# Kernel tuning notes

Hardware: AMD Instinct MI355X
Metric: run time of the kernel (lower is better)

Reference implementation:

```python
import jax, jax.numpy as jnp
import numpy as np

N, E, H, R = 32768, 524288, 128, 64
INV_SQRT_3 = 1.0 / np.sqrt(3.0)
INV_SQRT_H = 1.0 / np.sqrt(float(H))
INV_SQRT_2 = 1.0 / np.sqrt(2.0)


def scaled_silu(x):
    return jax.nn.silu(x) * (1.0 / 0.6)


def setup_inputs() -> dict:
    key = jax.random.key(0)
    ks = jax.random.split(key, 16)
    s = 0.05
    return {
        "x": jax.random.normal(ks[0], (N, H), jnp.float32),
        "vec": jax.random.normal(ks[1], (N, 3, H), jnp.float32),
        "edge_index": jax.random.randint(ks[2], (2, E), 0, N),
        "edge_embed": jax.random.normal(ks[3], (E, R), jnp.float32),
        "edge_vec": jax.random.normal(ks[4], (E, 3), jnp.float32),
        # message layer params
        "ln_g": jnp.ones((H,), jnp.float32),
        "ln_b": jnp.zeros((H,), jnp.float32),
        "W1": jax.random.normal(ks[5], (H, H), jnp.float32) * s,
        "b1": jnp.zeros((H,), jnp.float32),
        "W2": jax.random.normal(ks[6], (H, 3 * H), jnp.float32) * s,
        "b2": jnp.zeros((3 * H,), jnp.float32),
        "Wr": jax.random.normal(ks[7], (R, 3 * H), jnp.float32) * s,
        "br": jnp.zeros((3 * H,), jnp.float32),
        # update layer params
        "Wv": jax.random.normal(ks[8], (H, 2 * H), jnp.float32) * s,
        "Wu1": jax.random.normal(ks[9], (2 * H, H), jnp.float32) * s,
        "bu1": jnp.zeros((H,), jnp.float32),
        "Wu2": jax.random.normal(ks[10], (H, 3 * H), jnp.float32) * s,
        "bu2": jnp.zeros((3 * H,), jnp.float32),
    }


def _layernorm(x, g, b, eps=1e-5):
    mu = jnp.mean(x, axis=-1, keepdims=True)
    var = jnp.mean((x - mu) ** 2, axis=-1, keepdims=True)
    return (x - mu) * jax.lax.rsqrt(var + eps) * g + b


def _painn(x, vec, edge_index, edge_embed, edge_vec,
           ln_g, ln_b, W1, b1, W2, b2, Wr, br, Wv, Wu1, bu1, Wu2, bu2):
    src, dst = edge_index[0], edge_index[1]
    # --- message ---
    xh = scaled_silu(_layernorm(x, ln_g, ln_b) @ W1 + b1) @ W2 + b2  # [N,3H]
    rbfh = edge_embed @ Wr + br                                       # [E,3H]
    m = xh[src] * rbfh                                                # [E,3H]
    xh1, xh2, xh3 = jnp.split(m, 3, axis=-1)
    xh2 = xh2 * INV_SQRT_3
    vec_msg = (vec[src] * xh2[:, None, :] + xh3[:, None, :] * edge_vec[:, :, None]) * INV_SQRT_H  # [E,3,H]
    dx = jax.ops.segment_sum(xh1, dst, num_segments=N)
    dvec = jax.ops.segment_sum(vec_msg, dst, num_segments=N)
    x = (x + dx) * INV_SQRT_2
    vec = vec + dvec
    # --- update ---
    vproj = jnp.einsum('nch,hk->nck', vec, Wv)  # [N,3,2H]
    vec1, vec2 = jnp.split(vproj, 2, axis=-1)
    vec_dot = jnp.sum(vec1 * vec2, axis=1) * INV_SQRT_H  # [N,H]
    vec2_norm = jnp.sqrt(jnp.sum(vec2 ** 2, axis=-2) + 1e-8)  # [N,H]
    h = scaled_silu(jnp.concatenate([x, vec2_norm], axis=-1) @ Wu1 + bu1) @ Wu2 + bu2
    xv1, xv2, xv3 = jnp.split(h, 3, axis=-1)
    dx = (xv1 + xv2 * vec_dot) * INV_SQRT_2
    dvec = xv3[:, None, :] * vec1
    return vec + dvec, x + dx


def reference(x, vec, edge_index, edge_embed, edge_vec,
              ln_g, ln_b, W1, b1, W2, b2, Wr, br, Wv, Wu1, bu1, Wu2, bu2):
    return _painn(x, vec, edge_index, edge_embed, edge_vec,
                  ln_g, ln_b, W1, b1, W2, b2, Wr, br, Wv, Wu1, bu1, Wu2, bu2)
```

## Files before the change

### kernel.cpp

```cpp
#include <hip/hip_runtime.h>
#include <cstdint>
#include <cstddef>

#define NN 32768
#define NE 524288
#define H  128
#define H3 384
#define RB 64
#define EB 16
#define NPB 4
#define EEST 72
#define MSTRIDE 388
#define AST 136

#define INV_SQRT_3 0.5773502691896258f
#define INV_SQRT_H 0.08838834764831845f
#define INV_SQRT_2 0.7071067811865476f

typedef __attribute__((ext_vector_type(8))) short short8;
typedef __attribute__((ext_vector_type(4))) float f32x4;

__device__ __forceinline__ float scaled_silu(float v) {
    return v * (1.0f / 0.6f) / (1.0f + __expf(-v));
}
__device__ __forceinline__ short f2bf(float f) {
    uint32_t u = __float_as_uint(f);
    uint32_t r = (u + 0x7FFFu + ((u >> 16) & 1u)) >> 16;
    return (short)r;
}
__device__ __forceinline__ float bf2f(short s) {
    return __uint_as_float(((uint32_t)(uint16_t)s) << 16);
}

__global__ __launch_bounds__(256) void cvtT_kernel(const float* __restrict__ W,
        short* __restrict__ WT, int K, int M) {
    int i = blockIdx.x * 256 + threadIdx.x;
    int k = i / M, m = i % M;
    WT[(size_t)m * K + k] = f2bf(W[(size_t)k * M + m]);
}

__global__ __launch_bounds__(256) void veccvt_kernel(const float* __restrict__ v,
        short* __restrict__ vb) {
    int i = blockIdx.x * 256 + threadIdx.x;
    float4 a = ((const float4*)v)[i];
    short4 s4; s4.x = f2bf(a.x); s4.y = f2bf(a.y); s4.z = f2bf(a.z); s4.w = f2bf(a.w);
    ((short4*)vb)[i] = s4;
}

__global__ __launch_bounds__(256) void ln_kernel(const float* __restrict__ x,
        const float* __restrict__ g, const float* __restrict__ b,
        float* __restrict__ t) {
    int row  = blockIdx.x * 4 + (threadIdx.x >> 6);
    int lane = threadIdx.x & 63;
    const float* xr = x + (size_t)row * H;
    float v0 = xr[lane], v1 = xr[lane + 64];
    float s = v0 + v1;
#pragma unroll
    for (int off = 32; off; off >>= 1) s += __shfl_xor(s, off, 64);
    float mu = s * (1.0f / 128.0f);
    float d0 = v0 - mu, d1 = v1 - mu;
    float q = d0 * d0 + d1 * d1;
#pragma unroll
    for (int off = 32; off; off >>= 1) q += __shfl_xor(q, off, 64);
    float rs = rsqrtf(q * (1.0f / 128.0f) + 1e-5f);
    float* tr = t + (size_t)row * H;
    tr[lane]      = d0 * rs * g[lane]      + b[lane];
    tr[lane + 64] = d1 * rs * g[lane + 64] + b[lane + 64];
}

__global__ __launch_bounds__(256) void g1_mfma(const float* __restrict__ t,
        const short* __restrict__ W1T, const float* __restrict__ b1,
        short* __restrict__ h1_bf) {
    __shared__ short A_l[64 * AST];
    __shared__ short B_l[128 * AST];
    int tid = threadIdx.x;
    int w = tid >> 6, l = tid & 63, lm = l & 15, q = l >> 4;
    int r0 = blockIdx.x * 64;
    const float4* ag = (const float4*)(t + (size_t)r0 * H);
#pragma unroll
    for (int i = 0; i < 8; ++i) {
        int idx = tid + 256 * i;
        float4 a = ag[idx];
        int row = idx >> 5, c4 = idx & 31;
        short4 s4; s4.x = f2bf(a.x); s4.y = f2bf(a.y); s4.z = f2bf(a.z); s4.w = f2bf(a.w);
        *(short4*)&A_l[row * AST + c4 * 4] = s4;
    }
    const short8* wg = (const short8*)W1T;
#pragma unroll
    for (int i = 0; i < 8; ++i) {
        int idx = tid + 256 * i;
        int row = idx >> 4, c8 = idx & 15;
        *(short8*)&B_l[row * AST + c8 * 8] = wg[idx];
    }
    __syncthreads();
    short8 bf[2][4];
#pragma unroll
    for (int c = 0; c < 2; ++c)
#pragma unroll
        for (int ks = 0; ks < 4; ++ks)
            bf[c][ks] = *(const short8*)&B_l[((2 * w + c) * 16 + lm) * AST + ks * 32 + q * 8];
    f32x4 acc[4][2];
#pragma unroll
    for (int rt = 0; rt < 4; ++rt) { acc[rt][0] = (f32x4){0.f,0.f,0.f,0.f}; acc[rt][1] = (f32x4){0.f,0.f,0.f,0.f}; }
#pragma unroll
    for (int ks = 0; ks < 4; ++ks)
#pragma unroll
        for (int rt = 0; rt < 4; ++rt) {
            short8 a = *(const short8*)&A_l[(rt * 16 + lm) * AST + ks * 32 + q * 8];
            acc[rt][0] = __builtin_amdgcn_mfma_f32_16x16x32_bf16(a, bf[0][ks], acc[rt][0], 0, 0, 0);
            acc[rt][1] = __builtin_amdgcn_mfma_f32_16x16x32_bf16(a, bf[1][ks], acc[rt][1], 0, 0, 0);
        }
#pragma unroll
    for (int c = 0; c < 2; ++c) {
        int col = (2 * w + c) * 16 + lm;
        float bb = b1[col];
#pragma unroll
        for (int rt = 0; rt < 4; ++rt)
#pragma unroll
            for (int r = 0; r < 4; ++r) {
                int R = r0 + rt * 16 + q * 4 + r;
                h1_bf[(size_t)R * H + col] = f2bf(scaled_silu(acc[rt][c][r] + bb));
            }
    }
}

__global__ __launch_bounds__(256) void g2_mfma(const short* __restrict__ h1_bf,
        const short* __restrict__ W2T, const float* __restrict__ b2,
        short* __restrict__ xh_bf) {
    __shared__ short A_l[64 * AST];
    __shared__ short B_l[128 * AST];
    int tid = threadIdx.x;
    int w = tid >> 6, l = tid & 63, lm = l & 15, q = l >> 4;
    int r0 = blockIdx.x * 64;
    const short8* ag = (const short8*)(h1_bf + (size_t)r0 * H);
#pragma unroll
    for (int i = 0; i < 4; ++i) {
        int idx = tid + 256 * i;
        int row = idx >> 4, c8 = idx & 15;
        *(short8*)&A_l[row * AST + c8 * 8] = ag[idx];
    }
    for (int s = 0; s < 3; ++s) {
        __syncthreads();
        const short8* wg = (const short8*)(W2T + (size_t)s * 128 * 128);
#pragma unroll
        for (int i = 0; i < 8; ++i) {
            int idx = tid + 256 * i;
            int row = idx >> 4, c8 = idx & 15;
            *(short8*)&B_l[row * AST + c8 * 8] = wg[idx];
        }
        __syncthreads();
        short8 bf[2][4];
#pragma unroll
        for (int c = 0; c < 2; ++c)
#pragma unroll
            for (int ks = 0; ks < 4; ++ks)
                bf[c][ks] = *(const short8*)&B_l[((2 * w + c) * 16 + lm) * AST + ks * 32 + q * 8];
        f32x4 acc[4][2];
#pragma unroll
        for (int rt = 0; rt < 4; ++rt) { acc[rt][0] = (f32x4){0.f,0.f,0.f,0.f}; acc[rt][1] = (f32x4){0.f,0.f,0.f,0.f}; }
#pragma unroll
        for (int ks = 0; ks < 4; ++ks)
#pragma unroll
            for (int rt = 0; rt < 4; ++rt) {
                short8 a = *(const short8*)&A_l[(rt * 16 + lm) * AST + ks * 32 + q * 8];
                acc[rt][0] = __builtin_amdgcn_mfma_f32_16x16x32_bf16(a, bf[0][ks], acc[rt][0], 0, 0, 0);
                acc[rt][1] = __builtin_amdgcn_mfma_f32_16x16x32_bf16(a, bf[1][ks], acc[rt][1], 0, 0, 0);
            }
#pragma unroll
        for (int c = 0; c < 2; ++c) {
            int col = (2 * w + c) * 16 + lm;
            float bb = b2[s * H + col];
#pragma unroll
            for (int rt = 0; rt < 4; ++rt)
#pragma unroll
                for (int r = 0; r < 4; ++r) {
                    int R = r0 + rt * 16 + q * 4 + r;
                    xh_bf[(size_t)R * H3 + s * H + col] = f2bf(acc[rt][c][r] + bb);
                }
        }
    }
}

__global__ __launch_bounds__(256) void hist_kernel(const int* __restrict__ eidx,
        int* __restrict__ hist) {
    int e = blockIdx.x * 256 + threadIdx.x;
    atomicAdd(&hist[eidx[NE + e]], 1);
}

__global__ __launch_bounds__(1024) void scan_kernel(const int* __restrict__ hist,
        int* __restrict__ row_ptr, int* __restrict__ cursor) {
    __shared__ int sc[1024];
    int t = threadIdx.x;
    int base = t * 32;
    int v[32];
    int s = 0;
#pragma unroll
    for (int i = 0; i < 32; ++i) {
        int tmp = hist[base + i];
        v[i] = s;
        s += tmp;
    }
    sc[t] = s;
    __syncthreads();
    for (int off = 1; off < 1024; off <<= 1) {
        int a = sc[t];
        int b = (t >= off) ? sc[t - off] : 0;
        __syncthreads();
        sc[t] = a + b;
        __syncthreads();
    }
    int excl = sc[t] - s;
#pragma unroll
    for (int i = 0; i < 32; ++i) {
        int val = excl + v[i];
        row_ptr[base + i] = val;
        cursor[base + i] = val;
    }
    if (t == 0) row_ptr[32768] = NE;
}

__global__ __launch_bounds__(256) void scatter_kernel(const int* __restrict__ eidx,
        const float* __restrict__ evec, int* __restrict__ cursor,
        int* __restrict__ perm, int* __restrict__ srcs_s, int* __restrict__ dsts_s,
        float* __restrict__ ev_s) {
    int e = blockIdx.x * 256 + threadIdx.x;
    int d = eidx[NE + e];
    int pos = atomicAdd(&cursor[d], 1);
    perm[pos]   = e;
    srcs_s[pos] = eidx[e];
    dsts_s[pos] = d;
    ev_s[pos * 3 + 0] = evec[e * 3 + 0];
    ev_s[pos * 3 + 1] = evec[e * 3 + 1];
    ev_s[pos * 3 + 2] = evec[e * 3 + 2];
}

__global__ __launch_bounds__(256) void wrt_kernel(const float* __restrict__ Wr,
        short* __restrict__ WrT16) {
    int i = blockIdx.x * 256 + threadIdx.x;
    int n = i >> 6, k = i & 63;
    WrT16[i] = f2bf(Wr[(size_t)k * H3 + n]);
}

__global__ __launch_bounds__(384) void edge_mfma_kernel(
        const int* __restrict__ row_ptr, const int* __restrict__ perm,
        const int* __restrict__ srcs_s, const int* __restrict__ dsts_s,
        const float* __restrict__ ev_s, const float* __restrict__ eembed,
        const short* __restrict__ WrT16, const float* __restrict__ br,
        const short* __restrict__ xh_bf, const short* __restrict__ vec_bf,
        float* __restrict__ dx_out, float* __restrict__ dvec_out) {
    __shared__ float accdx[NPB * H];
    __shared__ float accdv[NPB * H3];
    __shared__ short eeL[EB * EEST];
    __shared__ float mst[EB * MSTRIDE];
    __shared__ int   sSrc[EB];
    __shared__ int   sLd[EB];
    __shared__ float sEv[EB][3];
    int j = threadIdx.x;
    int w = j >> 6, l = j & 63;
    int lm = l & 15, q = l >> 4;
    short8 bfrag[4][2];
#pragma unroll
    for (int t = 0; t < 4; ++t)
#pragma unroll
        for (int hf = 0; hf < 2; ++hf)
            bfrag[t][hf] = *(const short8*)(WrT16 +
                ((size_t)(w * 64 + t * 16 + lm) * 64 + q * 8 + hf * 32));
    float brj[4];
#pragma unroll
    for (int t = 0; t < 4; ++t) brj[t] = br[w * 64 + t * 16 + lm];
    float scale = (w < 2) ? 1.0f : ((w < 4) ? (INV_SQRT_3 * INV_SQRT_H) : INV_SQRT_H);
    int n0 = blockIdx.x * NPB;
    for (int i = j; i < NPB * H;  i += 384) accdx[i] = 0.f;
    for (int i = j; i < NPB * H3; i += 384) accdv[i] = 0.f;
    int ib = row_ptr[n0], ie = row_ptr[n0 + NPB];
    int c = j >> 7, hh = j & 127;
    __syncthreads();
    for (int base = ib; base < ie; base += EB) {
        int cnt = min(EB, ie - base);
        if (j < 256) {
            int e = j >> 4, c4 = j & 15;
            int i = base + ((e < cnt) ? e : 0);
            int p = perm[i];
            float4 a = ((const float4*)(eembed + (size_t)p * RB))[c4];
            short4 b4;
            b4.x = f2bf(a.x); b4.y = f2bf(a.y); b4.z = f2bf(a.z); b4.w = f2bf(a.w);
            *(short4*)(eeL + e * EEST + c4 * 4) = b4;
        }
        if (j < EB) {
            int i = base + ((j < cnt) ? j : 0);
            sSrc[j] = srcs_s[i];
            sLd[j]  = dsts_s[i] - n0;
            sEv[j][0] = ev_s[(size_t)i * 3 + 0];
            sEv[j][1] = ev_s[(size_t)i * 3 + 1];
            sEv[j][2] = ev_s[(size_t)i * 3 + 2];
        }
        __syncthreads();
        short xg[4][4];
#pragma unroll
        for (int r = 0; r < 4; ++r) {
            const short* xr = xh_bf + (size_t)sSrc[q * 4 + r] * H3 + w * 64 + lm;
#pragma unroll
            for (int t = 0; t < 4; ++t) xg[r][t] = xr[t * 16];
        }
        short vv[EB];
#pragma unroll
        for (int e = 0; e < EB; ++e)
            vv[e] = vec_bf[(size_t)sSrc[e] * H3 + j];
        short8 a0 = *(const short8*)(eeL + lm * EEST + q * 8);
        short8 a1 = *(const short8*)(eeL + lm * EEST + 32 + q * 8);
        f32x4 d[4];
#pragma unroll
        for (int t = 0; t < 4; ++t) {
            d[t] = __builtin_amdgcn_mfma_f32_16x16x32_bf16(a0, bfrag[t][0],
                       (f32x4){0.f, 0.f, 0.f, 0.f}, 0, 0, 0);
            d[t] = __builtin_amdgcn_mfma_f32_16x16x32_bf16(a1, bfrag[t][1], d[t], 0, 0, 0);
        }
#pragma unroll
        for (int r = 0; r < 4; ++r) {
            int e = q * 4 + r;
#pragma unroll
            for (int t = 0; t < 4; ++t) {
                float m = (d[t][r] + brj[t]) * bf2f(xg[r][t]) * scale;
                mst[e * MSTRIDE + w * 64 + t * 16 + lm] = m;
            }
        }
        __syncthreads();
        int cur = -1; float dva = 0.f, dxa = 0.f;
#pragma unroll
        for (int e = 0; e < EB; ++e) {
            if (e < cnt) {
                float m2 = mst[e * MSTRIDE + H + hh];
                float m3 = mst[e * MSTRIDE + 2 * H + hh];
                int ld = sLd[e];
                if (ld != cur) {
                    if (cur >= 0) {
                        accdv[cur * H3 + j] += dva;
                        if (j < H) accdx[cur * H + j] += dxa;
                    }
                    cur = ld; dva = 0.f; dxa = 0.f;
                }
                dva += bf2f(vv[e]) * m2 + m3 * sEv[e][c];
                if (j < H) dxa += mst[e * MSTRIDE + j];
            }
        }
        if (cur >= 0) {
            accdv[cur * H3 + j] += dva;
            if (j < H) accdx[cur * H + j] += dxa;
        }
        __syncthreads();
    }
    for (int i = j; i < NPB * H;  i += 384) dx_out[(size_t)n0 * H + i]    = accdx[i];
    for (int i = j; i < NPB * H3; i += 384) dvec_out[(size_t)n0 * H3 + i] = accdv[i];
}

__global__ __launch_bounds__(256) void d1a_kernel(const float* __restrict__ x,
        const float* __restrict__ vec, float* __restrict__ B1, float* __restrict__ B2) {
    int i = blockIdx.x * 256 + threadIdx.x;
    float4 dv = ((float4*)B1)[i];
    float4 vv = ((const float4*)vec)[i];
    dv.x += vv.x; dv.y += vv.y; dv.z += vv.z; dv.w += vv.w;
    ((float4*)B1)[i] = dv;
    if (i < NN * H / 4) {
        float4 dx = ((float4*)B2)[i];
        float4 xx = ((const float4*)x)[i];
        dx.x = (xx.x + dx.x) * INV_SQRT_2; dx.y = (xx.y + dx.y) * INV_SQRT_2;
        dx.z = (xx.z + dx.z) * INV_SQRT_2; dx.w = (xx.w + dx.w) * INV_SQRT_2;
        ((float4*)B2)[i] = dx;
    }
}

__global__ __launch_bounds__(256) void d1_vproj(const float* __restrict__ vec_mid,
        const short* __restrict__ WvT, float* __restrict__ vec1,
        float* __restrict__ vdot, short* __restrict__ vnorm_bf) {
    __shared__ short A_l[48 * AST];
    __shared__ short B_l[128 * AST];
    __shared__ float T1[48 * 132];
    __shared__ float T2[48 * 132];
    int tid = threadIdx.x;
    int w = tid >> 6, l = tid & 63, lm = l & 15, q = l >> 4;
    int r0 = blockIdx.x * 48;
    const float4* ag = (const float4*)(vec_mid + (size_t)r0 * H);
#pragma unroll
    for (int i = 0; i < 6; ++i) {
        int idx = tid + 256 * i;
        float4 a = ag[idx];
        int row = idx >> 5, c4 = idx & 31;
        short4 s4; s4.x = f2bf(a.x); s4.y = f2bf(a.y); s4.z = f2bf(a.z); s4.w = f2bf(a.w);
        *(short4*)&A_l[row * AST + c4 * 4] = s4;
    }
    for (int s = 0; s < 2; ++s) {
        __syncthreads();
        const short8* wg = (const short8*)(WvT + (size_t)s * 128 * 128);
#pragma unroll
        for (int i = 0; i < 8; ++i) {
            int idx = tid + 256 * i;
            int row = idx >> 4, c8 = idx & 15;
            *(short8*)&B_l[row * AST + c8 * 8] = wg[idx];
        }
        __syncthreads();
        short8 bf[2][4];
#pragma unroll
        for (int c = 0; c < 2; ++c)
#pragma unroll
            for (int ks = 0; ks < 4; ++ks)
                bf[c][ks] = *(const short8*)&B_l[((2 * w + c) * 16 + lm) * AST + ks * 32 + q * 8];
        f32x4 acc[3][2];
#pragma unroll
        for (int rt = 0; rt < 3; ++rt) { acc[rt][0] = (f32x4){0.f,0.f,0.f,0.f}; acc[rt][1] = (f32x4){0.f,0.f,0.f,0.f}; }
#pragma unroll
        for (int ks = 0; ks < 4; ++ks)
#pragma unroll
            for (int rt = 0; rt < 3; ++rt) {
                short8 a = *(const short8*)&A_l[(rt * 16 + lm) * AST + ks * 32 + q * 8];
                acc[rt][0] = __builtin_amdgcn_mfma_f32_16x16x32_bf16(a, bf[0][ks], acc[rt][0], 0, 0, 0);
                acc[rt][1] = __builtin_amdgcn_mfma_f32_16x16x32_bf16(a, bf[1][ks], acc[rt][1], 0, 0, 0);
            }
        float* T = s ? T2 : T1;
#pragma unroll
        for (int c = 0; c < 2; ++c) {
            int col = (2 * w + c) * 16 + lm;
#pragma unroll
            for (int rt = 0; rt < 3; ++rt)
#pragma unroll
                for (int r = 0; r < 4; ++r) {
                    int lr = rt * 16 + q * 4 + r;
                    float v = acc[rt][c][r];
                    T[lr * 132 + col] = v;
                    if (s == 0) vec1[(size_t)(r0 + lr) * H + col] = v;
                }
        }
    }
    __syncthreads();
    int nb = blockIdx.x * 16;
#pragma unroll
    for (int i = 0; i < 8; ++i) {
        int p = tid + 256 * i;
        int k = p & 127, m = p >> 7;
        float d = 0.f, s2 = 0.f;
#pragma unroll
        for (int c = 0; c < 3; ++c) {
            float v1 = T1[(m * 3 + c) * 132 + k];
            float v2 = T2[(m * 3 + c) * 132 + k];
            d += v1 * v2; s2 += v2 * v2;
        }
        vdot[(size_t)(nb + m) * H + k] = d * INV_SQRT_H;
        vnorm_bf[(size_t)(nb + m) * H + k] = f2bf(sqrtf(s2 + 1e-8f));
    }
}

__global__ __launch_bounds__(256) void d2a_mfma(const float* __restrict__ xmid,
        const short* __restrict__ vnorm_bf, const short* __restrict__ Wu1T,
        const float* __restrict__ bu1, short* __restrict__ u_bf) {
    __shared__ short A_l[64 * AST];
    __shared__ short B_l[128 * AST];
    int tid = threadIdx.x;
    int w = tid >> 6, l = tid & 63, lm = l & 15, q = l >> 4;
    int r0 = blockIdx.x * 64;
    f32x4 acc[4][2];
#pragma unroll
    for (int rt = 0; rt < 4; ++rt) { acc[rt][0] = (f32x4){0.f,0.f,0.f,0.f}; acc[rt][1] = (f32x4){0.f,0.f,0.f,0.f}; }
    for (int kh = 0; kh < 2; ++kh) {
        __syncthreads();
        if (kh == 0) {
            const float4* ag = (const float4*)(xmid + (size_t)r0 * H);
#pragma unroll
            for (int i = 0; i < 8; ++i) {
                int idx = tid + 256 * i;
                float4 a = ag[idx];
                int row = idx >> 5, c4 = idx & 31;
                short4 s4; s4.x = f2bf(a.x); s4.y = f2bf(a.y); s4.z = f2bf(a.z); s4.w = f2bf(a.w);
                *(short4*)&A_l[row * AST + c4 * 4] = s4;
            }
        } else {
            const short8* ag = (const short8*)(vnorm_bf + (size_t)r0 * H);
#pragma unroll
            for (int i = 0; i < 4; ++i) {
                int idx = tid + 256 * i;
                int row = idx >> 4, c8 = idx & 15;
                *(short8*)&A_l[row * AST + c8 * 8] = ag[idx];
            }
        }
#pragma unroll
        for (int i = 0; i < 8; ++i) {
            int idx = tid + 256 * i;
            int row = idx >> 4, c8 = idx & 15;
            *(short8*)&B_l[row * AST + c8 * 8] = ((const short8*)Wu1T)[row * 32 + kh * 16 + c8];
        }
        __syncthreads();
        short8 bf[2][4];
#pragma unroll
        for (int c = 0; c < 2; ++c)
#pragma unroll
            for (int ks = 0; ks < 4; ++ks)
                bf[c][ks] = *(const short8*)&B_l[((2 * w + c) * 16 + lm) * AST + ks * 32 + q * 8];
#pragma unroll
        for (int ks = 0; ks < 4; ++ks)
#pragma unroll
            for (int rt = 0; rt < 4; ++rt) {
                short8 a = *(const short8*)&A_l[(rt * 16 + lm) * AST + ks * 32 + q * 8];
                acc[rt][0] = __builtin_amdgcn_mfma_f32_16x16x32_bf16(a, bf[0][ks], acc[rt][0], 0, 0, 0);
                acc[rt][1] = __builtin_amdgcn_mfma_f32_16x16x32_bf16(a, bf[1][ks], acc[rt][1], 0, 0, 0);
            }
    }
#pragma unroll
    for (int c = 0; c < 2; ++c) {
        int col = (2 * w + c) * 16 + lm;
        float bb = bu1[col];
#pragma unroll
        for (int rt = 0; rt < 4; ++rt)
#pragma unroll
            for (int r = 0; r < 4; ++r) {
                int R = r0 + rt * 16 + q * 4 + r;
                u_bf[(size_t)R * H + col] = f2bf(scaled_silu(acc[rt][c][r] + bb));
            }
    }
}

__global__ __launch_bounds__(256) void d2b_mfma(const short* __restrict__ u_bf,
        const short* __restrict__ Wu2T, const float* __restrict__ bu2,
        const float* __restrict__ vdot, const float* __restrict__ xmid,
        const float* __restrict__ vec_mid, const float* __restrict__ vec1,
        float* __restrict__ out) {
    __shared__ short A_l[64 * AST];
    __shared__ short B_l[128 * AST];
    int tid = threadIdx.x;
    int w = tid >> 6, l = tid & 63, lm = l & 15, q = l >> 4;
    int r0 = blockIdx.x * 64;
    float* out_vec = out;
    float* out_x = out + (size_t)NN * H3;
    const short8* ag = (const short8*)(u_bf + (size_t)r0 * H);
#pragma unroll
    for (int i = 0; i < 4; ++i) {
        int idx = tid + 256 * i;
        int row = idx >> 4, c8 = idx & 15;
        *(short8*)&A_l[row * AST + c8 * 8] = ag[idx];
    }
    short8 bf0[2][4], bf1[2][4];
    __syncthreads();
    {
        const short8* wg = (const short8*)Wu2T;
#pragma unroll
        for (int i = 0; i < 8; ++i) {
            int idx = tid + 256 * i;
            int row = idx >> 4, c8 = idx & 15;
            *(short8*)&B_l[row * AST + c8 * 8] = wg[idx];
        }
    }
    __syncthreads();
#pragma unroll
    for (int c = 0; c < 2; ++c)
#pragma unroll
        for (int ks = 0; ks < 4; ++ks)
            bf0[c][ks] = *(const short8*)&B_l[((2 * w + c) * 16 + lm) * AST + ks * 32 + q * 8];
    __syncthreads();
    {
        const short8* wg = (const short8*)(Wu2T + 128 * 128);
#pragma unroll
        for (int i = 0; i < 8; ++i) {
            int idx = tid + 256 * i;
            int row = idx >> 4, c8 = idx & 15;
            *(short8*)&B_l[row * AST + c8 * 8] = wg[idx];
        }
    }
    __syncthreads();
#pragma unroll
    for (int c = 0; c < 2; ++c)
#pragma unroll
        for (int ks = 0; ks < 4; ++ks)
            bf1[c][ks] = *(const short8*)&B_l[((2 * w + c) * 16 + lm) * AST + ks * 32 + q * 8];
    f32x4 acc0[4][2], acc1[4][2];
#pragma unroll
    for (int rt = 0; rt < 4; ++rt) {
        acc0[rt][0] = (f32x4){0.f,0.f,0.f,0.f}; acc0[rt][1] = (f32x4){0.f,0.f,0.f,0.f};
        acc1[rt][0] = (f32x4){0.f,0.f,0.f,0.f}; acc1[rt][1] = (f32x4){0.f,0.f,0.f,0.f};
    }
#pragma unroll
    for (int ks = 0; ks < 4; ++ks)
#pragma unroll
        for (int rt = 0; rt < 4; ++rt) {
            short8 a = *(const short8*)&A_l[(rt * 16 + lm) * AST + ks * 32 + q * 8];
            acc0[rt][0] = __builtin_amdgcn_mfma_f32_16x16x32_bf16(a, bf0[0][ks], acc0[rt][0], 0, 0, 0);
            acc0[rt][1] = __builtin_amdgcn_mfma_f32_16x16x32_bf16(a, bf0[1][ks], acc0[rt][1], 0, 0, 0);
            acc1[rt][0] = __builtin_amdgcn_mfma_f32_16x16x32_bf16(a, bf1[0][ks], acc1[rt][0], 0, 0, 0);
            acc1[rt][1] = __builtin_amdgcn_mfma_f32_16x16x32_bf16(a, bf1[1][ks], acc1[rt][1], 0, 0, 0);
        }
#pragma unroll
    for (int c = 0; c < 2; ++c) {
        int col = (2 * w + c) * 16 + lm;
        float bb0 = bu2[col], bb1 = bu2[H + col];
#pragma unroll
        for (int rt = 0; rt < 4; ++rt)
#pragma unroll
            for (int r = 0; r < 4; ++r) {
                int R = r0 + rt * 16 + q * 4 + r;
                float xv1 = acc0[rt][c][r] + bb0;
                float xv2 = acc1[rt][c][r] + bb1;
                float dx2 = (xv1 + xv2 * vdot[(size_t)R * H + col]) * INV_SQRT_2;
                out_x[(size_t)R * H + col] = xmid[(size_t)R * H + col] + dx2;
            }
    }
    __syncthreads();
    {
        const short8* wg = (const short8*)(Wu2T + 2 * 128 * 128);
#pragma unroll
        for (int i = 0; i < 8; ++i) {
            int idx = tid + 256 * i;
            int row = idx >> 4, c8 = idx & 15;
            *(short8*)&B_l[row * AST + c8 * 8] = wg[idx];
        }
    }
    __syncthreads();
#pragma unroll
    for (int c = 0; c < 2; ++c)
#pragma unroll
        for (int ks = 0; ks < 4; ++ks)
            bf0[c][ks] = *(const short8*)&B_l[((2 * w + c) * 16 + lm) * AST + ks * 32 + q * 8];
#pragma unroll
    for (int rt = 0; rt < 4; ++rt) { acc0[rt][0] = (f32x4){0.f,0.f,0.f,0.f}; acc0[rt][1] = (f32x4){0.f,0.f,0.f,0.f}; }
#pragma unroll
    for (int ks = 0; ks < 4; ++ks)
#pragma unroll
        for (int rt = 0; rt < 4; ++rt) {
            short8 a = *(const short8*)&A_l[(rt * 16 + lm) * AST + ks * 32 + q * 8];
            acc0[rt][0] = __builtin_amdgcn_mfma_f32_16x16x32_bf16(a, bf0[0][ks], acc0[rt][0], 0, 0, 0);
            acc0[rt][1] = __builtin_amdgcn_mfma_f32_16x16x32_bf16(a, bf0[1][ks], acc0[rt][1], 0, 0, 0);
        }
#pragma unroll
    for (int c = 0; c < 2; ++c) {
        int col = (2 * w + c) * 16 + lm;
        float bb2 = bu2[2 * H + col];
#pragma unroll
        for (int rt = 0; rt < 4; ++rt)
#pragma unroll
            for (int r = 0; r < 4; ++r) {
                int R = r0 + rt * 16 + q * 4 + r;
                float xv3 = acc0[rt][c][r] + bb2;
#pragma unroll
                for (int c3 = 0; c3 < 3; ++c3) {
                    size_t idx = (size_t)R * H3 + c3 * H + col;
                    out_vec[idx] = vec_mid[idx] + xv3 * vec1[idx];
                }
            }
    }
}

extern "C" void kernel_launch(void* const* d_in, const int* in_sizes, int n_in,
                              void* d_out, int out_size, void* d_ws, size_t ws_size,
                              hipStream_t stream) {
    const float* x    = (const float*)d_in[0];
    const float* vec  = (const float*)d_in[1];
    const int*   eidx = (const int*)d_in[2];
    const float* eemb = (const float*)d_in[3];
    const float* evec = (const float*)d_in[4];
    const float* lng  = (const float*)d_in[5];
    const float* lnb  = (const float*)d_in[6];
    const float* W1   = (const float*)d_in[7];
    const float* b1   = (const float*)d_in[8];
    const float* W2   = (const float*)d_in[9];
    const float* b2   = (const float*)d_in[10];
    const float* Wr   = (const float*)d_in[11];
    const float* br   = (const float*)d_in[12];
    const float* Wv   = (const float*)d_in[13];
    const float* Wu1  = (const float*)d_in[14];
    const float* bu1  = (const float*)d_in[15];
    const float* Wu2  = (const float*)d_in[16];
    const float* bu2  = (const float*)d_in[17];

    float* B0 = (float*)d_ws;
    float* B1 = B0 + (size_t)NN * H3;
    float* B2 = B1 + (size_t)NN * H3;
    float* B3 = B2 + (size_t)NN * H;
    float* B4 = B3 + (size_t)NN * H;
    short* B5 = (short*)(B4 + (size_t)NN * H);
    float* out = (float*)d_out;

    int* row_ptr = (int*)B4;
    int* cursor  = row_ptr + 32772;
    int* perm    = cursor + 32768;
    int* srcs_s  = perm + NE;
    int* dsts_s  = srcs_s + NE;
    float* ev_s  = (float*)(dsts_s + NE);
    short* WrT16 = (short*)(ev_s + (size_t)NE * 3);

    short* vec_bf = B5;
    short* W1T  = vec_bf + (size_t)NN * H3;
    short* W2T  = W1T + 128 * 128;
    short* WvT  = W2T + 128 * 384;
    short* Wu1T = WvT + 128 * 256;
    short* Wu2T = Wu1T + 256 * 128;

    short* xh_bf    = (short*)B0;
    short* h1_bf    = (short*)B3;
    short* vnorm_bf = (short*)B4;
    short* u_bf     = vnorm_bf + (size_t)NN * H;

    cvtT_kernel<<<64,  256, 0, stream>>>(W1,  W1T,  128, 128);
    cvtT_kernel<<<192, 256, 0, stream>>>(W2,  W2T,  128, 384);
    cvtT_kernel<<<128, 256, 0, stream>>>(Wv,  WvT,  128, 256);
    cvtT_kernel<<<128, 256, 0, stream>>>(Wu1, Wu1T, 256, 128);
    cvtT_kernel<<<192, 256, 0, stream>>>(Wu2, Wu2T, 128, 384);
    wrt_kernel<<<(H3 * RB) / 256, 256, 0, stream>>>(Wr, WrT16);
    veccvt_kernel<<<(NN * H3 / 4) / 256, 256, 0, stream>>>(vec, vec_bf);

    ln_kernel<<<NN / 4, 256, 0, stream>>>(x, lng, lnb, B2);
    g1_mfma<<<NN / 64, 256, 0, stream>>>(B2, W1T, b1, h1_bf);
    g2_mfma<<<NN / 64, 256, 0, stream>>>(h1_bf, W2T, b2, xh_bf);

    hipMemsetAsync(row_ptr, 0, 32768 * sizeof(int), stream);
    hist_kernel<<<NE / 256, 256, 0, stream>>>(eidx, row_ptr);
    scan_kernel<<<1, 1024, 0, stream>>>(row_ptr, row_ptr, cursor);
    scatter_kernel<<<NE / 256, 256, 0, stream>>>(eidx, evec, cursor, perm, srcs_s, dsts_s, ev_s);

    edge_mfma_kernel<<<NN / NPB, 384, 0, stream>>>(row_ptr, perm, srcs_s, dsts_s, ev_s,
                                                   eemb, WrT16, br, xh_bf, vec_bf, B2, B1);

    d1a_kernel<<<(NN * H3 / 4) / 256, 256, 0, stream>>>(x, vec, B1, B2);
    d1_vproj<<<(NN * 3) / 48, 256, 0, stream>>>(B1, WvT, B0, B3, vnorm_bf);
    d2a_mfma<<<NN / 64, 256, 0, stream>>>(B2, vnorm_bf, Wu1T, bu1, u_bf);
    d2b_mfma<<<NN / 64, 256, 0, stream>>>(u_bf, Wu2T, bu2, B3, B2, B1, B0, out);
}
```

Baseline: 907.0 us.

## Prefetch next edge batch in edge kernel and fuse residual epilogue

The edge kernel now loads the next batch's permutation indices, src/dst, edge vectors and edge embeddings into registers while the current batch's MFMA and scatter work runs. It commits them to shared memory after the end-of-iteration barrier, so the load at the top of each iteration no longer needs its own barrier. The residual add and scaling that d1a_kernel did for x and vec now happen in the edge kernel's final store, which removes one kernel launch and a full read-modify-write pass over both buffers. The cost is higher register pressure from holding prefetched values in a 384-thread block.

```diff
diff --git a/kernel.cpp b/kernel.cpp
--- a/kernel.cpp
+++ b/kernel.cpp
@@ -247,6 +247,7 @@
         const float* __restrict__ ev_s, const float* __restrict__ eembed,
         const short* __restrict__ WrT16, const float* __restrict__ br,
         const short* __restrict__ xh_bf, const short* __restrict__ vec_bf,
+        const float* __restrict__ xin, const float* __restrict__ vecin,
         float* __restrict__ dx_out, float* __restrict__ dvec_out) {
     __shared__ float accdx[NPB * H];
     __shared__ float accdv[NPB * H3];
@@ -274,12 +275,12 @@
     for (int i = j; i < NPB * H3; i += 384) accdv[i] = 0.f;
     int ib = row_ptr[n0], ie = row_ptr[n0 + NPB];
     int c = j >> 7, hh = j & 127;
-    __syncthreads();
-    for (int base = ib; base < ie; base += EB) {
-        int cnt = min(EB, ie - base);
+
+    if (ib < ie) {
+        int cnt0 = min(EB, ie - ib);
         if (j < 256) {
             int e = j >> 4, c4 = j & 15;
-            int i = base + ((e < cnt) ? e : 0);
+            int i = ib + ((e < cnt0) ? e : 0);
             int p = perm[i];
             float4 a = ((const float4*)(eembed + (size_t)p * RB))[c4];
             short4 b4;
@@ -287,14 +288,36 @@
             *(short4*)(eeL + e * EEST + c4 * 4) = b4;
         }
         if (j < EB) {
-            int i = base + ((j < cnt) ? j : 0);
+            int i = ib + ((j < cnt0) ? j : 0);
             sSrc[j] = srcs_s[i];
             sLd[j]  = dsts_s[i] - n0;
             sEv[j][0] = ev_s[(size_t)i * 3 + 0];
             sEv[j][1] = ev_s[(size_t)i * 3 + 1];
             sEv[j][2] = ev_s[(size_t)i * 3 + 2];
         }
-        __syncthreads();
+    }
+
+    for (int base = ib; base < ie; base += EB) {
+        int cnt = min(EB, ie - base);
+        __syncthreads();
+        int nbase = base + EB;
+        int hn = nbase < ie;
+        int np = 0, msrc = 0, mdst = 0;
+        float me0 = 0.f, me1 = 0.f, me2 = 0.f;
+        if (hn) {
+            int cntn = min(EB, ie - nbase);
+            if (j < 256) {
+                int e = j >> 4;
+                np = perm[nbase + ((e < cntn) ? e : 0)];
+            }
+            if (j < EB) {
+                int i = nbase + ((j < cntn) ? j : 0);
+                msrc = srcs_s[i]; mdst = dsts_s[i];
+                me0 = ev_s[(size_t)i * 3 + 0];
+                me1 = ev_s[(size_t)i * 3 + 1];
+                me2 = ev_s[(size_t)i * 3 + 2];
+            }
+        }
         short xg[4][4];
 #pragma unroll
         for (int r = 0; r < 4; ++r) {
@@ -314,6 +337,11 @@
             d[t] = __builtin_amdgcn_mfma_f32_16x16x32_bf16(a0, bfrag[t][0],
                        (f32x4){0.f, 0.f, 0.f, 0.f}, 0, 0, 0);
             d[t] = __builtin_amdgcn_mfma_f32_16x16x32_bf16(a1, bfrag[t][1], d[t], 0, 0, 0);
+        }
+        float4 ereg;
+        if (hn && j < 256) {
+            int c4 = j & 15;
+            ereg = ((const float4*)(eembed + (size_t)np * RB))[c4];
         }
 #pragma unroll
         for (int r = 0; r < 4; ++r) {
@@ -348,25 +376,24 @@
             if (j < H) accdx[cur * H + j] += dxa;
         }
         __syncthreads();
-    }
-    for (int i = j; i < NPB * H;  i += 384) dx_out[(size_t)n0 * H + i]    = accdx[i];
-    for (int i = j; i < NPB * H3; i += 384) dvec_out[(size_t)n0 * H3 + i] = accdv[i];
-}
-
-__global__ __launch_bounds__(256) void d1a_kernel(const float* __restrict__ x,
-        const float* __restrict__ vec, float* __restrict__ B1, float* __restrict__ B2) {
-    int i = blockIdx.x * 256 + threadIdx.x;
-    float4 dv = ((float4*)B1)[i];
-    float4 vv = ((const float4*)vec)[i];
-    dv.x += vv.x; dv.y += vv.y; dv.z += vv.z; dv.w += vv.w;
-    ((float4*)B1)[i] = dv;
-    if (i < NN * H / 4) {
-        float4 dx = ((float4*)B2)[i];
-        float4 xx = ((const float4*)x)[i];
-        dx.x = (xx.x + dx.x) * INV_SQRT_2; dx.y = (xx.y + dx.y) * INV_SQRT_2;
-        dx.z = (xx.z + dx.z) * INV_SQRT_2; dx.w = (xx.w + dx.w) * INV_SQRT_2;
-        ((float4*)B2)[i] = dx;
-    }
+        if (hn) {
+            if (j < 256) {
+                int e = j >> 4, c4 = j & 15;
+                short4 b4;
+                b4.x = f2bf(ereg.x); b4.y = f2bf(ereg.y);
+                b4.z = f2bf(ereg.z); b4.w = f2bf(ereg.w);
+                *(short4*)(eeL + e * EEST + c4 * 4) = b4;
+            }
+            if (j < EB) {
+                sSrc[j] = msrc; sLd[j] = mdst - n0;
+                sEv[j][0] = me0; sEv[j][1] = me1; sEv[j][2] = me2;
+            }
+        }
+    }
+    for (int i = j; i < NPB * H;  i += 384)
+        dx_out[(size_t)n0 * H + i] = (xin[(size_t)n0 * H + i] + accdx[i]) * INV_SQRT_2;
+    for (int i = j; i < NPB * H3; i += 384)
+        dvec_out[(size_t)n0 * H3 + i] = vecin[(size_t)n0 * H3 + i] + accdv[i];
 }
 
 __global__ __launch_bounds__(256) void d1_vproj(const float* __restrict__ vec_mid,
@@ -712,9 +739,9 @@
     scatter_kernel<<<NE / 256, 256, 0, stream>>>(eidx, evec, cursor, perm, srcs_s, dsts_s, ev_s);
 
     edge_mfma_kernel<<<NN / NPB, 384, 0, stream>>>(row_ptr, perm, srcs_s, dsts_s, ev_s,
-                                                   eemb, WrT16, br, xh_bf, vec_bf, B2, B1);
-
-    d1a_kernel<<<(NN * H3 / 4) / 256, 256, 0, stream>>>(x, vec, B1, B2);
+                                                   eemb, WrT16, br, xh_bf, vec_bf,
+                                                   x, vec, B2, B1);
+
     d1_vproj<<<(NN * 3) / 48, 256, 0, stream>>>(B1, WvT, B0, B3, vnorm_bf);
     d2a_mfma<<<NN / 64, 256, 0, stream>>>(B2, vnorm_bf, Wu1T, bu1, u_bf);
     d2b_mfma<<<NN / 64, 256, 0, stream>>>(u_bf, Wu2T, bu2, B3, B2, B1, B0, out);
```

Result: slower. 1.020 ms (+12.4%).

## Pre-gather edge embeddings in sorted bf16 order and fuse residual adds

Applied to the files above, without the earlier changes.

Adds a kernel that permutes edge_embed into destination-sorted order and converts it to bf16 in a scratch buffer (aliasing the output). The edge kernel then loads contiguous bf16 rows instead of gathering fp32 rows through perm. The separate residual-add kernel is removed, and its x/vec additions are folded into the edge kernel's final store. This trades an extra streaming pass for coalesced loads and one fewer full-tensor read/write pass.

```diff
diff --git a/kernel.cpp b/kernel.cpp
--- a/kernel.cpp
+++ b/kernel.cpp
@@ -234,6 +234,20 @@
     ev_s[pos * 3 + 2] = evec[e * 3 + 2];
 }
 
+__global__ __launch_bounds__(256) void eegather_kernel(const int* __restrict__ perm,
+        const float* __restrict__ eembed, short* __restrict__ ee_s) {
+    int idx = blockIdx.x * 256 + threadIdx.x;
+    int pos = idx >> 3, t = idx & 7;
+    int e = perm[pos];
+    const float4* src = (const float4*)(eembed + (size_t)e * RB);
+    float4 a = src[t * 2];
+    float4 b = src[t * 2 + 1];
+    short8 s;
+    s[0] = f2bf(a.x); s[1] = f2bf(a.y); s[2] = f2bf(a.z); s[3] = f2bf(a.w);
+    s[4] = f2bf(b.x); s[5] = f2bf(b.y); s[6] = f2bf(b.z); s[7] = f2bf(b.w);
+    ((short8*)(ee_s + (size_t)pos * RB))[t] = s;
+}
+
 __global__ __launch_bounds__(256) void wrt_kernel(const float* __restrict__ Wr,
         short* __restrict__ WrT16) {
     int i = blockIdx.x * 256 + threadIdx.x;
@@ -242,11 +256,12 @@
 }
 
 __global__ __launch_bounds__(384) void edge_mfma_kernel(
-        const int* __restrict__ row_ptr, const int* __restrict__ perm,
+        const int* __restrict__ row_ptr,
         const int* __restrict__ srcs_s, const int* __restrict__ dsts_s,
-        const float* __restrict__ ev_s, const float* __restrict__ eembed,
+        const float* __restrict__ ev_s, const short* __restrict__ ee_s,
         const short* __restrict__ WrT16, const float* __restrict__ br,
         const short* __restrict__ xh_bf, const short* __restrict__ vec_bf,
+        const float* __restrict__ xin, const float* __restrict__ vecin,
         float* __restrict__ dx_out, float* __restrict__ dvec_out) {
     __shared__ float accdx[NPB * H];
     __shared__ float accdv[NPB * H3];
@@ -277,14 +292,11 @@
     __syncthreads();
     for (int base = ib; base < ie; base += EB) {
         int cnt = min(EB, ie - base);
-        if (j < 256) {
-            int e = j >> 4, c4 = j & 15;
+        if (j < 128) {
+            int e = j >> 3, c8 = j & 7;
             int i = base + ((e < cnt) ? e : 0);
-            int p = perm[i];
-            float4 a = ((const float4*)(eembed + (size_t)p * RB))[c4];
-            short4 b4;
-            b4.x = f2bf(a.x); b4.y = f2bf(a.y); b4.z = f2bf(a.z); b4.w = f2bf(a.w);
-            *(short4*)(eeL + e * EEST + c4 * 4) = b4;
+            *(short8*)(eeL + e * EEST + c8 * 8) =
+                ((const short8*)ee_s)[(size_t)i * 8 + c8];
         }
         if (j < EB) {
             int i = base + ((j < cnt) ? j : 0);
@@ -349,24 +361,10 @@
         }
         __syncthreads();
     }
-    for (int i = j; i < NPB * H;  i += 384) dx_out[(size_t)n0 * H + i]    = accdx[i];
-    for (int i = j; i < NPB * H3; i += 384) dvec_out[(size_t)n0 * H3 + i] = accdv[i];
-}
-
-__global__ __launch_bounds__(256) void d1a_kernel(const float* __restrict__ x,
-        const float* __restrict__ vec, float* __restrict__ B1, float* __restrict__ B2) {
-    int i = blockIdx.x * 256 + threadIdx.x;
-    float4 dv = ((float4*)B1)[i];
-    float4 vv = ((const float4*)vec)[i];
-    dv.x += vv.x; dv.y += vv.y; dv.z += vv.z; dv.w += vv.w;
-    ((float4*)B1)[i] = dv;
-    if (i < NN * H / 4) {
-        float4 dx = ((float4*)B2)[i];
-        float4 xx = ((const float4*)x)[i];
-        dx.x = (xx.x + dx.x) * INV_SQRT_2; dx.y = (xx.y + dx.y) * INV_SQRT_2;
-        dx.z = (xx.z + dx.z) * INV_SQRT_2; dx.w = (xx.w + dx.w) * INV_SQRT_2;
-        ((float4*)B2)[i] = dx;
-    }
+    for (int i = j; i < NPB * H;  i += 384)
+        dx_out[(size_t)n0 * H + i] = (xin[(size_t)n0 * H + i] + accdx[i]) * INV_SQRT_2;
+    for (int i = j; i < NPB * H3; i += 384)
+        dvec_out[(size_t)n0 * H3 + i] = vecin[(size_t)n0 * H3 + i] + accdv[i];
 }
 
 __global__ __launch_bounds__(256) void d1_vproj(const float* __restrict__ vec_mid,
@@ -673,6 +671,7 @@
     float* B4 = B3 + (size_t)NN * H;
     short* B5 = (short*)(B4 + (size_t)NN * H);
     float* out = (float*)d_out;
+    short* ee_s = (short*)d_out;
 
     int* row_ptr = (int*)B4;
     int* cursor  = row_ptr + 32772;
@@ -710,11 +709,12 @@
     hist_kernel<<<NE / 256, 256, 0, stream>>>(eidx, row_ptr);
     scan_kernel<<<1, 1024, 0, stream>>>(row_ptr, row_ptr, cursor);
     scatter_kernel<<<NE / 256, 256, 0, stream>>>(eidx, evec, cursor, perm, srcs_s, dsts_s, ev_s);
-
-    edge_mfma_kernel<<<NN / NPB, 384, 0, stream>>>(row_ptr, perm, srcs_s, dsts_s, ev_s,
-                                                   eemb, WrT16, br, xh_bf, vec_bf, B2, B1);
-
-    d1a_kernel<<<(NN * H3 / 4) / 256, 256, 0, stream>>>(x, vec, B1, B2);
+    eegather_kernel<<<(NE * 8) / 256, 256, 0, stream>>>(perm, eemb, ee_s);
+
+    edge_mfma_kernel<<<NN / NPB, 384, 0, stream>>>(row_ptr, srcs_s, dsts_s, ev_s,
+                                                   ee_s, WrT16, br, xh_bf, vec_bf,
+                                                   x, vec, B2, B1);
+
     d1_vproj<<<(NN * 3) / 48, 256, 0, stream>>>(B1, WvT, B0, B3, vnorm_bf);
     d2a_mfma<<<NN / 64, 256, 0, stream>>>(B2, vnorm_bf, Wu1T, bu1, u_bf);
     d2b_mfma<<<NN / 64, 256, 0, stream>>>(u_bf, Wu2T, bu2, B3, B2, B1, B0, out);
```

Measured after the change: 937.0 us. 3.3% more time.
